# Kernel tuning notes

Measured on AMD Instinct MI355X. Metric: run time of the kernel, lower is better.

The kernel has to match this reference:

```python
import jax, jax.numpy as jnp
import numpy as np

N = 8192
E = 524288
IN_DIM = 128
HID = 256
OUT_DIM = 128
N_LAYERS = 3
N_HEADS = 4
HEAD_DIM = HID // N_HEADS


def setup_inputs() -> dict:
    key = jax.random.key(0)
    ks = jax.random.split(key, 12)
    s = 0.05
    return {
        "x": jax.random.normal(ks[0], (N, IN_DIM), dtype=jnp.float32),
        "edge_index": jax.random.randint(ks[1], (2, E), 0, N, dtype=jnp.int64),
        "W_in": jax.random.normal(ks[2], (HID, IN_DIM), dtype=jnp.float32) * s,
        "b_in": jnp.zeros((HID,), dtype=jnp.float32),
        "plasticity": jnp.ones((N_LAYERS,), dtype=jnp.float32),
        "synaptic": jnp.ones((N_LAYERS,), dtype=jnp.float32),
        "in_proj_w": jax.random.normal(ks[3], (3 * HID, HID), dtype=jnp.float32) * s,
        "in_proj_b": jnp.zeros((3 * HID,), dtype=jnp.float32),
        "out_proj_w": jax.random.normal(ks[4], (HID, HID), dtype=jnp.float32) * s,
        "out_proj_b": jnp.zeros((HID,), dtype=jnp.float32),
        "W_out": jax.random.normal(ks[5], (OUT_DIM, HID), dtype=jnp.float32) * s,
        "b_out": jnp.zeros((OUT_DIM,), dtype=jnp.float32),
    }


def _forward(x, edge_index, W_in, b_in, plasticity, synaptic,
             in_proj_w, in_proj_b, out_proj_w, out_proj_b, W_out, b_out):
    src, dst = edge_index[0], edge_index[1]  # x_j = x[src], aggregate at dst (source_to_target)
    x = x @ W_in.T + b_in  # [N, HID]
    for i in range(N_LAYERS):
        x = x * jax.nn.sigmoid(plasticity[i])
        # message: x_j * sigmoid(synaptic) (scalar edge weight); aggr='add'
        agg = jax.ops.segment_sum(x[src], dst, num_segments=N)  # gather-scatter-add
        x = jax.nn.leaky_relu(agg * jax.nn.sigmoid(synaptic[i]), negative_slope=0.01)
    # MultiheadAttention over all N nodes (seq_len=N, batch=1)
    qkv = x @ in_proj_w.T + in_proj_b  # [N, 3*HID]
    q, k, v = jnp.split(qkv, 3, axis=-1)
    q = q.reshape(N, N_HEADS, HEAD_DIM).transpose(1, 0, 2)  # [h, n, d]
    k = k.reshape(N, N_HEADS, HEAD_DIM).transpose(1, 0, 2)
    v = v.reshape(N, N_HEADS, HEAD_DIM).transpose(1, 0, 2)
    scores = jnp.einsum("hnd,hmd->hnm", q, k) / np.sqrt(HEAD_DIM).astype(np.float32)
    attn = jax.nn.softmax(scores, axis=-1)
    o = jnp.einsum("hnm,hmd->hnd", attn, v)  # [h, n, d]
    o = o.transpose(1, 0, 2).reshape(N, HID)
    x = o @ out_proj_w.T + out_proj_b
    return x @ W_out.T + b_out  # [N, OUT_DIM]


def reference(x, edge_index, W_in, b_in, plasticity, synaptic,
              in_proj_w, in_proj_b, out_proj_w, out_proj_b, W_out, b_out):
    return _forward(x, edge_index, W_in, b_in, plasticity, synaptic,
                    in_proj_w, in_proj_b, out_proj_w, out_proj_b, W_out, b_out)
```

## Files before the change

kernel.cpp:

```cpp
#include <hip/hip_runtime.h>
#include <hip/hip_bf16.h>
#include <float.h>

#define N_NODES 8192
#define NEDGE   524288
#define IND     128
#define HID     256
#define OUTD    128
#define NHEAD   4
#define HD      64

typedef short short8 __attribute__((ext_vector_type(8)));
typedef float f32x4  __attribute__((ext_vector_type(4)));
typedef float f32x16 __attribute__((ext_vector_type(16)));
typedef unsigned int u32x4 __attribute__((ext_vector_type(4)));

__device__ __forceinline__ float sigmoidf_(float x) { return 1.0f / (1.0f + expf(-x)); }

__device__ __forceinline__ unsigned short f2bf(float f) {
    __hip_bfloat16 b = __float2bfloat16(f);
    return __builtin_bit_cast(unsigned short, b);
}
__device__ __forceinline__ float bf2f(unsigned short u) {
    __hip_bfloat16 b = __builtin_bit_cast(__hip_bfloat16, u);
    return __bfloat162float(b);
}
__device__ __forceinline__ void split3(float x, unsigned short& a, unsigned short& b, unsigned short& c) {
    a = f2bf(x); float r = x - bf2f(a);
    b = f2bf(r); r = r - bf2f(b);
    c = f2bf(r);
}
__device__ __forceinline__ unsigned int cvtpk(float lo, float hi) {
    unsigned int r;
    asm("v_cvt_pk_bf16_f32 %0, %1, %2" : "=v"(r) : "v"(lo), "v"(hi));
    return r;
}
__device__ __forceinline__ void plswap(unsigned int& a, unsigned int& b) {
    asm volatile("v_permlane32_swap_b32 %0, %1" : "+v"(a), "+v"(b));
}
__device__ __forceinline__ void gll16(const void* g, void* l) {
    __builtin_amdgcn_global_load_lds(
        (const __attribute__((address_space(1))) void*)g,
        (__attribute__((address_space(3))) void*)l, 16, 0, 0);
}
__device__ __forceinline__ f32x16 mfma32(short8 a, short8 b, f32x16 c) {
    return __builtin_amdgcn_mfma_f32_32x32x16_bf16(a, b, c, 0, 0, 0);
}

__global__ __launch_bounds__(256) void gemm_bias_kernel(
    const float* __restrict__ A, const float* __restrict__ W,
    const float* __restrict__ bias, float* __restrict__ C,
    int M, int Nn, int K)
{
    __shared__ float As[128][33];
    __shared__ float Ws[64][33];
    const int t  = threadIdx.x;
    const int tx = t & 15, ty = t >> 4;
    const int m0 = blockIdx.x * 128, n0 = blockIdx.y * 64;
    const int alr = t >> 1, alc = (t & 1) * 16;
    const int wlr = t >> 2, wlc = (t & 3) * 8;

    float acc[8][4] = {};
    for (int kk = 0; kk < K; kk += 32) {
        const float* Ap = A + (size_t)(m0 + alr) * K + kk + alc;
        const float* Wp = W + (size_t)(n0 + wlr) * K + kk + wlc;
        float4 a0 = *(const float4*)(Ap);
        float4 a1 = *(const float4*)(Ap + 4);
        float4 a2 = *(const float4*)(Ap + 8);
        float4 a3 = *(const float4*)(Ap + 12);
        float4 w0 = *(const float4*)(Wp);
        float4 w1 = *(const float4*)(Wp + 4);
        __syncthreads();
        *(float4*)(&As[alr][alc + 0])  = a0;
        *(float4*)(&As[alr][alc + 4])  = a1;
        *(float4*)(&As[alr][alc + 8])  = a2;
        *(float4*)(&As[alr][alc + 12]) = a3;
        *(float4*)(&Ws[wlr][wlc + 0])  = w0;
        *(float4*)(&Ws[wlr][wlc + 4])  = w1;
        __syncthreads();
        #pragma unroll 4
        for (int k = 0; k < 32; ++k) {
            float a[8], w[4];
            #pragma unroll
            for (int i = 0; i < 8; ++i) a[i] = As[ty * 8 + i][k];
            #pragma unroll
            for (int j = 0; j < 4; ++j) w[j] = Ws[tx * 4 + j][k];
            #pragma unroll
            for (int i = 0; i < 8; ++i)
                #pragma unroll
                for (int j = 0; j < 4; ++j)
                    acc[i][j] += a[i] * w[j];
        }
    }
    #pragma unroll
    for (int i = 0; i < 8; ++i) {
        const int m = m0 + ty * 8 + i;
        #pragma unroll
        for (int j = 0; j < 4; ++j) {
            const int n = n0 + tx * 4 + j;
            C[(size_t)m * Nn + n] = acc[i][j] + bias[n];
        }
    }
}

__global__ void hist_kernel(const int* __restrict__ ei, int* __restrict__ deg)
{
    int e = blockIdx.x * blockDim.x + threadIdx.x;
    if (e < NEDGE) atomicAdd(&deg[ei[NEDGE + e]], 1);
}

__global__ __launch_bounds__(1024) void scan_kernel(
    const int* __restrict__ deg, int* __restrict__ row_ptr, int* __restrict__ cursor)
{
    __shared__ int sh[1024];
    const int t = threadIdx.x;
    int v[8]; int s = 0;
    #pragma unroll
    for (int i = 0; i < 8; ++i) { v[i] = deg[t * 8 + i]; s += v[i]; }
    sh[t] = s; __syncthreads();
    for (int off = 1; off < 1024; off <<= 1) {
        int add = (t >= off) ? sh[t - off] : 0;
        __syncthreads();
        sh[t] += add;
        __syncthreads();
    }
    int base = sh[t] - s;
    #pragma unroll
    for (int i = 0; i < 8; ++i) {
        row_ptr[t * 8 + i] = base;
        cursor[t * 8 + i]  = base;
        base += v[i];
    }
    if (t == 1023) row_ptr[N_NODES] = base;
}

__global__ void scatter_kernel(const int* __restrict__ ei, int* __restrict__ cursor,
                               int* __restrict__ esrc)
{
    int e = blockIdx.x * blockDim.x + threadIdx.x;
    if (e < NEDGE) {
        int d = ei[NEDGE + e];
        int p = atomicAdd(&cursor[d], 1);
        esrc[p] = ei[e];
    }
}

__global__ __launch_bounds__(256) void aggregate_kernel(
    const float* __restrict__ hin, float* __restrict__ hout,
    const int* __restrict__ row_ptr, const int* __restrict__ esrc,
    const float* __restrict__ plas, const float* __restrict__ syn, int layer)
{
    const int b = blockIdx.x;
    const int c = threadIdx.x;
    const int st = row_ptr[b], en = row_ptr[b + 1];
    float a0 = 0.f, a1 = 0.f, a2 = 0.f, a3 = 0.f;
    int e = st;
    for (; e + 4 <= en; e += 4) {
        int s0 = esrc[e], s1 = esrc[e + 1], s2 = esrc[e + 2], s3 = esrc[e + 3];
        a0 += hin[(size_t)s0 * HID + c];
        a1 += hin[(size_t)s1 * HID + c];
        a2 += hin[(size_t)s2 * HID + c];
        a3 += hin[(size_t)s3 * HID + c];
    }
    float acc = (a0 + a1) + (a2 + a3);
    for (; e < en; ++e) acc += hin[(size_t)esrc[e] * HID + c];
    const float scale = sigmoidf_(plas[layer]) * sigmoidf_(syn[layer]);
    float x = acc * scale;
    hout[(size_t)b * HID + c] = (x > 0.f) ? x : 0.01f * x;
}

__global__ __launch_bounds__(256) void split_kernel(
    const float* __restrict__ qkv,
    unsigned short* __restrict__ Kc0, unsigned short* __restrict__ Kc1,
    unsigned short* __restrict__ Kc2, unsigned short* __restrict__ Vt0)
{
    __shared__ unsigned short vts[64 * 80];
    const int h  = blockIdx.y;
    const int n0 = blockIdx.x * 64;
    const int t  = threadIdx.x;
    const int r  = t >> 2;
    const int n  = n0 + r;
    const int dc = (t & 3) * 16;

    {
        const float* kp = qkv + (size_t)n * 768 + 256 + h * 64 + dc;
        float kv[16];
        #pragma unroll
        for (int i = 0; i < 16; i += 4) {
            float4 f = *(const float4*)(kp + i);
            kv[i] = f.x; kv[i+1] = f.y; kv[i+2] = f.z; kv[i+3] = f.w;
        }
        #pragma unroll
        for (int half = 0; half < 2; ++half) {
            short8 c0, c1, c2;
            #pragma unroll
            for (int j = 0; j < 8; ++j) {
                unsigned short a, b, c;
                split3(kv[half * 8 + j], a, b, c);
                c0[j] = (short)a; c1[j] = (short)b; c2[j] = (short)c;
            }
            const int pos = ((dc >> 3) + half) ^ (n & 7);
            const size_t base = ((size_t)(h * 8192 + n)) * 64 + pos * 8;
            *(short8*)(Kc0 + base) = c0;
            *(short8*)(Kc1 + base) = c1;
            *(short8*)(Kc2 + base) = c2;
        }
    }
    {
        const float* vp = qkv + (size_t)n * 768 + 512 + h * 64 + dc;
        #pragma unroll
        for (int i = 0; i < 16; i += 4) {
            float4 f = *(const float4*)(vp + i);
            float vv[4] = {f.x, f.y, f.z, f.w};
            #pragma unroll
            for (int k2 = 0; k2 < 4; ++k2)
                vts[(dc + i + k2) * 80 + r] = f2bf(vv[k2]);
        }
    }
    __syncthreads();
    #pragma unroll
    for (int i = 0; i < 2; ++i) {
        const int q = t * 2 + i;
        const int d = q >> 3, nc = q & 7;
        short8 vv = *(const short8*)(&vts[d * 80 + nc * 8]);
        const size_t dst = ((size_t)(h * 64 + d)) * 8192 + n0 + ((nc ^ (d & 7)) * 8);
        *(short8*)(Vt0 + dst) = vv;
    }
}

__global__ __launch_bounds__(256, 2) void attn_mfma_kernel(
    const float* __restrict__ qkv,
    const unsigned short* __restrict__ Kc0, const unsigned short* __restrict__ Kc1,
    const unsigned short* __restrict__ Kc2, const unsigned short* __restrict__ Vt0,
    unsigned short* __restrict__ Op16, float* __restrict__ Ml)
{
    __shared__ __align__(16) char smem[65536];
    const int h    = blockIdx.y;
    const int quar = blockIdx.z;
    const int n0   = blockIdx.x * 256;
    const int t    = threadIdx.x;
    const int wv   = t >> 6;
    const int lane = t & 63;
    const int l31  = lane & 31, l5 = lane >> 5;
    const int qbase = n0 + wv * 64;

    short8 qf[2][3][4];
    #pragma unroll
    for (int qb = 0; qb < 2; ++qb) {
        #pragma unroll
        for (int ks = 0; ks < 4; ++ks) {
            const float* qp = qkv + (size_t)(qbase + qb * 32 + l31) * 768 + h * 64 + ks * 16 + l5 * 8;
            float4 qa = *(const float4*)qp, qb4 = *(const float4*)(qp + 4);
            float qv[8] = {qa.x, qa.y, qa.z, qa.w, qb4.x, qb4.y, qb4.z, qb4.w};
            #pragma unroll
            for (int j = 0; j < 8; ++j) {
                unsigned short a, b, c;
                split3(qv[j] * 0.125f, a, b, c);
                qf[qb][0][ks][j] = (short)a;
                qf[qb][1][ks][j] = (short)b;
                qf[qb][2][ks][j] = (short)c;
            }
        }
    }

    const unsigned short* cbase = (wv == 0) ? Kc0 : (wv == 1) ? Kc1 : (wv == 2) ? Kc2 : Vt0;
    const char* sgb[8];
    #pragma unroll
    for (int s = 0; s < 8; ++s) {
        const int row = s * 8 + (lane >> 3);
        if (wv < 3)
            sgb[s] = (const char*)(cbase + ((size_t)(h * 8192 + row)) * 64 + (lane & 7) * 8);
        else
            sgb[s] = (const char*)(cbase + ((size_t)(h * 64 + row)) * 8192 + (lane & 7) * 8);
    }
    const size_t ktstride = (wv < 3) ? 8192 : 128;
    const int ldsbase = wv * 8192;

    auto STAGE = [&](int ktg, int bb) {
        #pragma unroll
        for (int s = 0; s < 8; ++s)
            gll16(sgb[s] + (size_t)ktg * ktstride, &smem[bb * 32768 + ldsbase + s * 1024]);
    };

    f32x16 o[2][2];
    #pragma unroll
    for (int db = 0; db < 2; ++db)
        #pragma unroll
        for (int qb = 0; qb < 2; ++qb)
            #pragma unroll
            for (int r = 0; r < 16; ++r) o[db][qb][r] = 0.f;
    float mr[2] = {-FLT_MAX, -FLT_MAX};
    float ls[2] = {0.f, 0.f};

    const int kt0 = quar * 32;
    STAGE(kt0, 0);
    __syncthreads();

    for (int kt = 0; kt < 32; ++kt) {
        const int bb = kt & 1;
        if (kt < 31) STAGE(kt0 + kt + 1, bb ^ 1);
        const char* buf = &smem[bb * 32768];

        f32x16 s[2][2];
        #pragma unroll
        for (int kb = 0; kb < 2; ++kb)
            #pragma unroll
            for (int qb = 0; qb < 2; ++qb)
                #pragma unroll
                for (int r = 0; r < 16; ++r) s[kb][qb][r] = 0.f;

        __builtin_amdgcn_s_setprio(1);
        #pragma unroll
        for (int ks = 0; ks < 4; ++ks) {
            #pragma unroll
            for (int kb = 0; kb < 2; ++kb) {
                const int key = kb * 32 + l31;
                const int off = key * 128 + (((ks * 2 + l5) ^ (key & 7)) * 16);
                short8 k0 = *(const short8*)(buf + off);
                short8 k1 = *(const short8*)(buf + 8192 + off);
                short8 k2 = *(const short8*)(buf + 16384 + off);
                #pragma unroll
                for (int qb = 0; qb < 2; ++qb) {
                    f32x16 acc = s[kb][qb];
                    acc = mfma32(k0, qf[qb][2][ks], acc);
                    acc = mfma32(k1, qf[qb][1][ks], acc);
                    acc = mfma32(k2, qf[qb][0][ks], acc);
                    acc = mfma32(k0, qf[qb][1][ks], acc);
                    acc = mfma32(k1, qf[qb][0][ks], acc);
                    acc = mfma32(k0, qf[qb][0][ks], acc);
                    s[kb][qb] = acc;
                }
            }
        }
        __builtin_amdgcn_s_setprio(0);

        short8 pb[2][4];
        #pragma unroll
        for (int qb = 0; qb < 2; ++qb) {
            float mx = s[0][qb][0];
            #pragma unroll
            for (int r = 1; r < 16; ++r) mx = fmaxf(mx, s[0][qb][r]);
            #pragma unroll
            for (int r = 0; r < 16; ++r) mx = fmaxf(mx, s[1][qb][r]);
            mx = fmaxf(mx, __shfl_xor(mx, 32));
            if (__any(mx > mr[qb] + 8.f)) {
                const float mn = fmaxf(mr[qb], mx);
                const float alpha = __expf(mr[qb] - mn);
                mr[qb] = mn;
                ls[qb] *= alpha;
                o[0][qb] *= alpha;
                o[1][qb] *= alpha;
            }
            const float mkeep = mr[qb];
            float ps = 0.f;
            #pragma unroll
            for (int kb = 0; kb < 2; ++kb)
                #pragma unroll
                for (int r = 0; r < 16; ++r) {
                    float p = __expf(s[kb][qb][r] - mkeep);
                    s[kb][qb][r] = p;
                    ps += p;
                }
            ps += __shfl_xor(ps, 32);
            ls[qb] += ps;

            #pragma unroll
            for (int ks = 0; ks < 4; ++ks) {
                const int kb = ks >> 1, rb = (ks & 1) * 8;
                unsigned int A0 = cvtpk(s[kb][qb][rb + 0], s[kb][qb][rb + 1]);
                unsigned int A1 = cvtpk(s[kb][qb][rb + 2], s[kb][qb][rb + 3]);
                unsigned int B0 = cvtpk(s[kb][qb][rb + 4], s[kb][qb][rb + 5]);
                unsigned int B1 = cvtpk(s[kb][qb][rb + 6], s[kb][qb][rb + 7]);
                plswap(A0, B0);
                plswap(A1, B1);
                u32x4 pw; pw[0] = A0; pw[1] = A1; pw[2] = B0; pw[3] = B1;
                pb[qb][ks] = __builtin_bit_cast(short8, pw);
            }
        }

        __builtin_amdgcn_s_setprio(1);
        #pragma unroll
        for (int ks = 0; ks < 4; ++ks) {
            #pragma unroll
            for (int db = 0; db < 2; ++db) {
                const int d = db * 32 + l31;
                const int off = 24576 + d * 128 + (((ks * 2 + l5) ^ (d & 7)) * 16);
                short8 v = *(const short8*)(buf + off);
                o[db][0] = mfma32(v, pb[0][ks], o[db][0]);
                o[db][1] = mfma32(v, pb[1][ks], o[db][1]);
            }
        }
        __builtin_amdgcn_s_setprio(0);

        __syncthreads();
    }

    #pragma unroll
    for (int qb = 0; qb < 2; ++qb) {
        const int q = qbase + qb * 32 + l31;
        unsigned short* opq = Op16 + ((size_t)((quar * 4 + h) * 8192 + q)) * 64;
        #pragma unroll
        for (int db = 0; db < 2; ++db) {
            #pragma unroll
            for (int tq = 0; tq < 4; ++tq) {
                const int d0 = db * 32 + tq * 8 + l5 * 4;
                unsigned int w0 = cvtpk(o[db][qb][4 * tq + 0], o[db][qb][4 * tq + 1]);
                unsigned int w1 = cvtpk(o[db][qb][4 * tq + 2], o[db][qb][4 * tq + 3]);
                uint2 st = {w0, w1};
                *(uint2*)(opq + d0) = st;
            }
        }
        if (l5 == 0) {
            Ml[((size_t)(quar * 4 + h) * 2 + 0) * 8192 + q] = mr[qb];
            Ml[((size_t)(quar * 4 + h) * 2 + 1) * 8192 + q] = ls[qb];
        }
    }
}

__global__ __launch_bounds__(256) void combine_kernel(
    const unsigned short* __restrict__ Op16, const float* __restrict__ Ml,
    float* __restrict__ aO)
{
    const int idx = blockIdx.x * 256 + threadIdx.x;
    const int c = idx & 3;
    const int q = (idx >> 2) & 8191;
    const int h = idx >> 15;
    float m[4], l[4];
    float mg = -FLT_MAX;
    #pragma unroll
    for (int s = 0; s < 4; ++s) {
        m[s] = Ml[((size_t)(s * 4 + h) * 2 + 0) * 8192 + q];
        l[s] = Ml[((size_t)(s * 4 + h) * 2 + 1) * 8192 + q];
        mg = fmaxf(mg, m[s]);
    }
    float w[4], denom = 0.f;
    #pragma unroll
    for (int s = 0; s < 4; ++s) {
        w[s] = __expf(m[s] - mg);
        denom += l[s] * w[s];
    }
    const float inv = 1.f / denom;
    float acc[16] = {};
    #pragma unroll
    for (int s = 0; s < 4; ++s) {
        const unsigned short* p = Op16 + ((size_t)(s * 4 + h) * 8192 + q) * 64 + c * 16;
        short8 v0 = *(const short8*)(p);
        short8 v1 = *(const short8*)(p + 8);
        #pragma unroll
        for (int i = 0; i < 8; ++i) {
            acc[i]     += w[s] * bf2f((unsigned short)v0[i]);
            acc[i + 8] += w[s] * bf2f((unsigned short)v1[i]);
        }
    }
    float* dst = aO + (size_t)q * 256 + h * 64 + c * 16;
    #pragma unroll
    for (int i = 0; i < 4; ++i) {
        float4 r = { acc[4*i] * inv, acc[4*i+1] * inv, acc[4*i+2] * inv, acc[4*i+3] * inv };
        *(float4*)(dst + i * 4) = r;
    }
}

extern "C" void kernel_launch(void* const* d_in, const int* in_sizes, int n_in,
                              void* d_out, int out_size, void* d_ws, size_t ws_size,
                              hipStream_t stream)
{
    const float* x     = (const float*)d_in[0];
    const int*   ei    = (const int*)  d_in[1];
    const float* W_in  = (const float*)d_in[2];
    const float* b_in  = (const float*)d_in[3];
    const float* plas  = (const float*)d_in[4];
    const float* syn   = (const float*)d_in[5];
    const float* inpw  = (const float*)d_in[6];
    const float* inpb  = (const float*)d_in[7];
    const float* outpw = (const float*)d_in[8];
    const float* outpb = (const float*)d_in[9];
    const float* Wout  = (const float*)d_in[10];
    const float* bout  = (const float*)d_in[11];
    float* out = (float*)d_out;

    char* ws = (char*)d_ws;
    float* h    = (float*)(ws + 0);
    float* h2   = (float*)(ws + (8u  << 20));
    float* qkv  = (float*)(ws + (16u << 20));
    float* aO   = (float*)(ws + 0);
    float* tmp  = (float*)(ws + (48u << 20));
    unsigned short* Op16 = (unsigned short*)(ws + (40u << 20));
    unsigned short* Kc0 = (unsigned short*)(ws + 0);
    unsigned short* Kc1 = (unsigned short*)(ws + (4u  << 20));
    unsigned short* Kc2 = (unsigned short*)(ws + (8u  << 20));
    unsigned short* Vt0 = (unsigned short*)(ws + (12u << 20));
    int*   rowp = (int*)(ws + (56u << 20));
    int*   curs = (int*)(ws + (56u << 20) + 40960);
    int*   esrc = (int*)(ws + (56u << 20) + 81920);
    float* Ml   = (float*)(ws + (56u << 20) + 81920);

    hipMemsetAsync(curs, 0, N_NODES * sizeof(int), stream);
    hist_kernel<<<NEDGE / 256, 256, 0, stream>>>(ei, curs);
    scan_kernel<<<1, 1024, 0, stream>>>(curs, rowp, curs);
    scatter_kernel<<<NEDGE / 256, 256, 0, stream>>>(ei, curs, esrc);

    gemm_bias_kernel<<<dim3(N_NODES / 128, HID / 64), 256, 0, stream>>>(
        x, W_in, b_in, h, N_NODES, HID, IND);

    aggregate_kernel<<<N_NODES, 256, 0, stream>>>(h,  h2, rowp, esrc, plas, syn, 0);
    aggregate_kernel<<<N_NODES, 256, 0, stream>>>(h2, h,  rowp, esrc, plas, syn, 1);
    aggregate_kernel<<<N_NODES, 256, 0, stream>>>(h,  h2, rowp, esrc, plas, syn, 2);

    gemm_bias_kernel<<<dim3(N_NODES / 128, 768 / 64), 256, 0, stream>>>(
        h2, inpw, inpb, qkv, N_NODES, 768, HID);

    split_kernel<<<dim3(N_NODES / 64, NHEAD), 256, 0, stream>>>(
        qkv, Kc0, Kc1, Kc2, Vt0);

    attn_mfma_kernel<<<dim3(N_NODES / 256, NHEAD, 4), 256, 0, stream>>>(
        qkv, Kc0, Kc1, Kc2, Vt0, Op16, Ml);

    combine_kernel<<<512, 256, 0, stream>>>(Op16, Ml, aO);

    gemm_bias_kernel<<<dim3(N_NODES / 128, HID / 64), 256, 0, stream>>>(
        aO, outpw, outpb, tmp, N_NODES, HID, HID);
    gemm_bias_kernel<<<dim3(N_NODES / 128, OUTD / 64), 256, 0, stream>>>(
        tmp, Wout, bout, out, N_NODES, OUTD, HID);
}
```

Before: 590.1 us.

## Replace FP32 SIMT GEMMs with split-bf16 MFMA GEMMs and retile attention

Replaces the scalar FP32 GEMM kernel with an MFMA kernel that emulates FP32 through 3-way or 2-way bf16 splits, so the input, QKV, output-projection and final GEMMs run on matrix cores. The last aggregation, the combine step and the output projection now emit bf16 split components directly. The attention kernel is retiled to 128 queries per block with half the LDS, so three blocks fit per CU; it also uses exp2 with a folded log2e scale and a lazy max-rescale threshold. The V layout swizzle changes to match. The 2-term splits on the later GEMMs cost some accuracy, and the extra split passes add memory traffic.

```diff
diff --git a/kernel.cpp b/kernel.cpp
--- a/kernel.cpp
+++ b/kernel.cpp
@@ -11,6 +11,7 @@
 #define HD      64
 
 typedef short short8 __attribute__((ext_vector_type(8)));
+typedef short short4v __attribute__((ext_vector_type(4)));
 typedef float f32x4  __attribute__((ext_vector_type(4)));
 typedef float f32x16 __attribute__((ext_vector_type(16)));
 typedef unsigned int u32x4 __attribute__((ext_vector_type(4)));
@@ -30,6 +31,10 @@
     b = f2bf(r); r = r - bf2f(b);
     c = f2bf(r);
 }
+__device__ __forceinline__ void split2(float x, unsigned short& a, unsigned short& b) {
+    a = f2bf(x); float r = x - bf2f(a);
+    b = f2bf(r);
+}
 __device__ __forceinline__ unsigned int cvtpk(float lo, float hi) {
     unsigned int r;
     asm("v_cvt_pk_bf16_f32 %0, %1, %2" : "=v"(r) : "v"(lo), "v"(hi));
@@ -45,62 +50,6 @@
 }
 __device__ __forceinline__ f32x16 mfma32(short8 a, short8 b, f32x16 c) {
     return __builtin_amdgcn_mfma_f32_32x32x16_bf16(a, b, c, 0, 0, 0);
-}
-
-__global__ __launch_bounds__(256) void gemm_bias_kernel(
-    const float* __restrict__ A, const float* __restrict__ W,
-    const float* __restrict__ bias, float* __restrict__ C,
-    int M, int Nn, int K)
-{
-    __shared__ float As[128][33];
-    __shared__ float Ws[64][33];
-    const int t  = threadIdx.x;
-    const int tx = t & 15, ty = t >> 4;
-    const int m0 = blockIdx.x * 128, n0 = blockIdx.y * 64;
-    const int alr = t >> 1, alc = (t & 1) * 16;
-    const int wlr = t >> 2, wlc = (t & 3) * 8;
-
-    float acc[8][4] = {};
-    for (int kk = 0; kk < K; kk += 32) {
-        const float* Ap = A + (size_t)(m0 + alr) * K + kk + alc;
-        const float* Wp = W + (size_t)(n0 + wlr) * K + kk + wlc;
-        float4 a0 = *(const float4*)(Ap);
-        float4 a1 = *(const float4*)(Ap + 4);
-        float4 a2 = *(const float4*)(Ap + 8);
-        float4 a3 = *(const float4*)(Ap + 12);
-        float4 w0 = *(const float4*)(Wp);
-        float4 w1 = *(const float4*)(Wp + 4);
-        __syncthreads();
-        *(float4*)(&As[alr][alc + 0])  = a0;
-        *(float4*)(&As[alr][alc + 4])  = a1;
-        *(float4*)(&As[alr][alc + 8])  = a2;
-        *(float4*)(&As[alr][alc + 12]) = a3;
-        *(float4*)(&Ws[wlr][wlc + 0])  = w0;
-        *(float4*)(&Ws[wlr][wlc + 4])  = w1;
-        __syncthreads();
-        #pragma unroll 4
-        for (int k = 0; k < 32; ++k) {
-            float a[8], w[4];
-            #pragma unroll
-            for (int i = 0; i < 8; ++i) a[i] = As[ty * 8 + i][k];
-            #pragma unroll
-            for (int j = 0; j < 4; ++j) w[j] = Ws[tx * 4 + j][k];
-            #pragma unroll
-            for (int i = 0; i < 8; ++i)
-                #pragma unroll
-                for (int j = 0; j < 4; ++j)
-                    acc[i][j] += a[i] * w[j];
-        }
-    }
-    #pragma unroll
-    for (int i = 0; i < 8; ++i) {
-        const int m = m0 + ty * 8 + i;
-        #pragma unroll
-        for (int j = 0; j < 4; ++j) {
-            const int n = n0 + tx * 4 + j;
-            C[(size_t)m * Nn + n] = acc[i][j] + bias[n];
-        }
-    }
 }
 
 __global__ void hist_kernel(const int* __restrict__ ei, int* __restrict__ deg)
@@ -143,6 +92,27 @@
         int p = atomicAdd(&cursor[d], 1);
         esrc[p] = ei[e];
     }
+}
+
+__global__ __launch_bounds__(256) void split_x_kernel(
+    const float* __restrict__ x,
+    unsigned short* __restrict__ X0, unsigned short* __restrict__ X1,
+    unsigned short* __restrict__ X2)
+{
+    const int i = (blockIdx.x * 256 + threadIdx.x) * 8;
+    float4 a = *(const float4*)(x + i);
+    float4 b = *(const float4*)(x + i + 4);
+    float v[8] = {a.x, a.y, a.z, a.w, b.x, b.y, b.z, b.w};
+    short8 c0, c1, c2;
+    #pragma unroll
+    for (int j = 0; j < 8; ++j) {
+        unsigned short p, q, r;
+        split3(v[j], p, q, r);
+        c0[j] = (short)p; c1[j] = (short)q; c2[j] = (short)r;
+    }
+    *(short8*)(X0 + i) = c0;
+    *(short8*)(X1 + i) = c1;
+    *(short8*)(X2 + i) = c2;
 }
 
 __global__ __launch_bounds__(256) void aggregate_kernel(
@@ -167,6 +137,117 @@
     const float scale = sigmoidf_(plas[layer]) * sigmoidf_(syn[layer]);
     float x = acc * scale;
     hout[(size_t)b * HID + c] = (x > 0.f) ? x : 0.01f * x;
+}
+
+__global__ __launch_bounds__(256) void aggregate_split_kernel(
+    const float* __restrict__ hin,
+    unsigned short* __restrict__ H0, unsigned short* __restrict__ H1,
+    unsigned short* __restrict__ H2,
+    const int* __restrict__ row_ptr, const int* __restrict__ esrc,
+    const float* __restrict__ plas, const float* __restrict__ syn, int layer)
+{
+    const int b = blockIdx.x;
+    const int c = threadIdx.x;
+    const int st = row_ptr[b], en = row_ptr[b + 1];
+    float a0 = 0.f, a1 = 0.f, a2 = 0.f, a3 = 0.f;
+    int e = st;
+    for (; e + 4 <= en; e += 4) {
+        int s0 = esrc[e], s1 = esrc[e + 1], s2 = esrc[e + 2], s3 = esrc[e + 3];
+        a0 += hin[(size_t)s0 * HID + c];
+        a1 += hin[(size_t)s1 * HID + c];
+        a2 += hin[(size_t)s2 * HID + c];
+        a3 += hin[(size_t)s3 * HID + c];
+    }
+    float acc = (a0 + a1) + (a2 + a3);
+    for (; e < en; ++e) acc += hin[(size_t)esrc[e] * HID + c];
+    const float scale = sigmoidf_(plas[layer]) * sigmoidf_(syn[layer]);
+    float x = acc * scale;
+    x = (x > 0.f) ? x : 0.01f * x;
+    unsigned short p, q, r;
+    split3(x, p, q, r);
+    H0[(size_t)b * HID + c] = p;
+    H1[(size_t)b * HID + c] = q;
+    H2[(size_t)b * HID + c] = r;
+}
+
+template<int NT, int NA, bool SOUT>
+__global__ __launch_bounds__(256) void mfma_gemm_kernel(
+    const unsigned short* __restrict__ A0, const unsigned short* __restrict__ A1,
+    const unsigned short* __restrict__ A2,
+    const float* __restrict__ W, const float* __restrict__ bias,
+    float* __restrict__ Cf, unsigned short* __restrict__ C0, unsigned short* __restrict__ C1,
+    int M, int Nn, int K)
+{
+    const int t = threadIdx.x;
+    const int wv = t >> 6, lane = t & 63;
+    const int l31 = lane & 31, l5 = lane >> 5;
+    const int wm = wv & 1, wn = wv >> 1;
+    const int m0 = blockIdx.x * 64 + wm * 32;
+    const int n0 = blockIdx.y * 64 + wn * 32;
+    const int mrow = m0 + l31;
+    const int nrow = n0 + l31;
+
+    f32x16 o;
+    #pragma unroll
+    for (int r = 0; r < 16; ++r) o[r] = 0.f;
+
+    for (int k = 0; k < K; k += 16) {
+        const int kk = k + l5 * 8;
+        short8 af[NA];
+        af[0] = *(const short8*)(A0 + (size_t)mrow * K + kk);
+        af[1] = *(const short8*)(A1 + (size_t)mrow * K + kk);
+        if (NA > 2) af[2] = *(const short8*)(A2 + (size_t)mrow * K + kk);
+        const float* wp = W + (size_t)nrow * K + kk;
+        float4 w4a = *(const float4*)wp, w4b = *(const float4*)(wp + 4);
+        float wvle[8] = {w4a.x, w4a.y, w4a.z, w4a.w, w4b.x, w4b.y, w4b.z, w4b.w};
+        short8 wf[3];
+        #pragma unroll
+        for (int j = 0; j < 8; ++j) {
+            if (NT == 6) {
+                unsigned short a, b, c;
+                split3(wvle[j], a, b, c);
+                wf[0][j] = (short)a; wf[1][j] = (short)b; wf[2][j] = (short)c;
+            } else {
+                unsigned short a, b;
+                split2(wvle[j], a, b);
+                wf[0][j] = (short)a; wf[1][j] = (short)b;
+            }
+        }
+        if (NT == 6) {
+            o = mfma32(wf[0], af[2], o);
+            o = mfma32(wf[1], af[1], o);
+            o = mfma32(wf[2], af[0], o);
+            o = mfma32(wf[0], af[1], o);
+            o = mfma32(wf[1], af[0], o);
+            o = mfma32(wf[0], af[0], o);
+        } else {
+            o = mfma32(wf[0], af[1], o);
+            o = mfma32(wf[1], af[0], o);
+            o = mfma32(wf[0], af[0], o);
+        }
+    }
+
+    #pragma unroll
+    for (int g = 0; g < 4; ++g) {
+        const int nb = n0 + g * 8 + l5 * 4;
+        const float4 b4 = *(const float4*)(bias + nb);
+        float v0 = o[4 * g + 0] + b4.x;
+        float v1 = o[4 * g + 1] + b4.y;
+        float v2 = o[4 * g + 2] + b4.z;
+        float v3 = o[4 * g + 3] + b4.w;
+        if (!SOUT) {
+            float4 st = {v0, v1, v2, v3};
+            *(float4*)(Cf + (size_t)mrow * Nn + nb) = st;
+        } else {
+            unsigned short h0, h1, p0, p1, q0, q1, r0, r1;
+            split2(v0, h0, h1); split2(v1, p0, p1);
+            split2(v2, q0, q1); split2(v3, r0, r1);
+            short4v s0 = {(short)h0, (short)p0, (short)q0, (short)r0};
+            short4v s1 = {(short)h1, (short)p1, (short)q1, (short)r1};
+            *(short4v*)(C0 + (size_t)mrow * Nn + nb) = s0;
+            *(short4v*)(C1 + (size_t)mrow * Nn + nb) = s1;
+        }
+    }
 }
 
 __global__ __launch_bounds__(256) void split_kernel(
@@ -222,172 +303,152 @@
     for (int i = 0; i < 2; ++i) {
         const int q = t * 2 + i;
         const int d = q >> 3, nc = q & 7;
+        const int g = nc >> 2, c = nc & 3;
         short8 vv = *(const short8*)(&vts[d * 80 + nc * 8]);
-        const size_t dst = ((size_t)(h * 64 + d)) * 8192 + n0 + ((nc ^ (d & 7)) * 8);
+        const size_t dst = ((size_t)(h * 64 + d)) * 8192 + n0 + g * 32 + ((c ^ (d & 3)) * 8);
         *(short8*)(Vt0 + dst) = vv;
     }
 }
 
-__global__ __launch_bounds__(256, 2) void attn_mfma_kernel(
+__global__ __launch_bounds__(256, 3) void attn_mfma_kernel(
     const float* __restrict__ qkv,
     const unsigned short* __restrict__ Kc0, const unsigned short* __restrict__ Kc1,
     const unsigned short* __restrict__ Kc2, const unsigned short* __restrict__ Vt0,
     unsigned short* __restrict__ Op16, float* __restrict__ Ml)
 {
-    __shared__ __align__(16) char smem[65536];
+    __shared__ __align__(16) char smem[32768];
     const int h    = blockIdx.y;
     const int quar = blockIdx.z;
-    const int n0   = blockIdx.x * 256;
+    const int n0   = blockIdx.x * 128;
     const int t    = threadIdx.x;
     const int wv   = t >> 6;
     const int lane = t & 63;
     const int l31  = lane & 31, l5 = lane >> 5;
-    const int qbase = n0 + wv * 64;
-
-    short8 qf[2][3][4];
-    #pragma unroll
-    for (int qb = 0; qb < 2; ++qb) {
+    const int qbase = n0 + wv * 32;
+
+    const float QSC = 0.125f * 1.4426950408889634f;
+    short8 qf[3][4];
+    #pragma unroll
+    for (int ks = 0; ks < 4; ++ks) {
+        const float* qp = qkv + (size_t)(qbase + l31) * 768 + h * 64 + ks * 16 + l5 * 8;
+        float4 qa = *(const float4*)qp, qb4 = *(const float4*)(qp + 4);
+        float qv[8] = {qa.x, qa.y, qa.z, qa.w, qb4.x, qb4.y, qb4.z, qb4.w};
+        #pragma unroll
+        for (int j = 0; j < 8; ++j) {
+            unsigned short a, b, c;
+            split3(qv[j] * QSC, a, b, c);
+            qf[0][ks][j] = (short)a;
+            qf[1][ks][j] = (short)b;
+            qf[2][ks][j] = (short)c;
+        }
+    }
+
+    const char* sgb[4];
+    int ldso[4];
+    #pragma unroll
+    for (int i = 0; i < 4; ++i) {
+        const int s = wv * 4 + i;
+        if (s < 12) {
+            const int c = s >> 2, rb = s & 3;
+            const unsigned short* base = (c == 0) ? Kc0 : (c == 1) ? Kc1 : Kc2;
+            const int row = rb * 8 + (lane >> 3);
+            sgb[i] = (const char*)(base + ((size_t)(h * 8192 + quar * 2048 + row)) * 64 + (lane & 7) * 8);
+            ldso[i] = c * 4096 + rb * 1024;
+        } else {
+            const int v = s - 12;
+            const int d = v * 16 + (lane >> 2);
+            sgb[i] = (const char*)(Vt0 + ((size_t)(h * 64 + d)) * 8192 + quar * 2048 + (lane & 3) * 8);
+            ldso[i] = 12288 + v * 1024;
+        }
+    }
+    const size_t ktstride = (wv < 3) ? 4096 : 64;
+
+    auto STAGE = [&](int kt, int bb) {
+        #pragma unroll
+        for (int i = 0; i < 4; ++i)
+            gll16(sgb[i] + (size_t)kt * ktstride, &smem[bb * 16384 + ldso[i]]);
+    };
+
+    f32x16 o[2];
+    #pragma unroll
+    for (int db = 0; db < 2; ++db)
+        #pragma unroll
+        for (int r = 0; r < 16; ++r) o[db][r] = 0.f;
+    float mr = -FLT_MAX, ls = 0.f;
+
+    STAGE(0, 0);
+    __syncthreads();
+
+    for (int kt = 0; kt < 64; ++kt) {
+        const int bb = kt & 1;
+        if (kt < 63) STAGE(kt + 1, bb ^ 1);
+        const char* buf = &smem[bb * 16384];
+
+        f32x16 s;
+        #pragma unroll
+        for (int r = 0; r < 16; ++r) s[r] = 0.f;
+
+        __builtin_amdgcn_s_setprio(1);
         #pragma unroll
         for (int ks = 0; ks < 4; ++ks) {
-            const float* qp = qkv + (size_t)(qbase + qb * 32 + l31) * 768 + h * 64 + ks * 16 + l5 * 8;
-            float4 qa = *(const float4*)qp, qb4 = *(const float4*)(qp + 4);
-            float qv[8] = {qa.x, qa.y, qa.z, qa.w, qb4.x, qb4.y, qb4.z, qb4.w};
-            #pragma unroll
-            for (int j = 0; j < 8; ++j) {
-                unsigned short a, b, c;
-                split3(qv[j] * 0.125f, a, b, c);
-                qf[qb][0][ks][j] = (short)a;
-                qf[qb][1][ks][j] = (short)b;
-                qf[qb][2][ks][j] = (short)c;
-            }
-        }
-    }
-
-    const unsigned short* cbase = (wv == 0) ? Kc0 : (wv == 1) ? Kc1 : (wv == 2) ? Kc2 : Vt0;
-    const char* sgb[8];
-    #pragma unroll
-    for (int s = 0; s < 8; ++s) {
-        const int row = s * 8 + (lane >> 3);
-        if (wv < 3)
-            sgb[s] = (const char*)(cbase + ((size_t)(h * 8192 + row)) * 64 + (lane & 7) * 8);
-        else
-            sgb[s] = (const char*)(cbase + ((size_t)(h * 64 + row)) * 8192 + (lane & 7) * 8);
-    }
-    const size_t ktstride = (wv < 3) ? 8192 : 128;
-    const int ldsbase = wv * 8192;
-
-    auto STAGE = [&](int ktg, int bb) {
-        #pragma unroll
-        for (int s = 0; s < 8; ++s)
-            gll16(sgb[s] + (size_t)ktg * ktstride, &smem[bb * 32768 + ldsbase + s * 1024]);
-    };
-
-    f32x16 o[2][2];
-    #pragma unroll
-    for (int db = 0; db < 2; ++db)
-        #pragma unroll
-        for (int qb = 0; qb < 2; ++qb)
-            #pragma unroll
-            for (int r = 0; r < 16; ++r) o[db][qb][r] = 0.f;
-    float mr[2] = {-FLT_MAX, -FLT_MAX};
-    float ls[2] = {0.f, 0.f};
-
-    const int kt0 = quar * 32;
-    STAGE(kt0, 0);
-    __syncthreads();
-
-    for (int kt = 0; kt < 32; ++kt) {
-        const int bb = kt & 1;
-        if (kt < 31) STAGE(kt0 + kt + 1, bb ^ 1);
-        const char* buf = &smem[bb * 32768];
-
-        f32x16 s[2][2];
-        #pragma unroll
-        for (int kb = 0; kb < 2; ++kb)
-            #pragma unroll
-            for (int qb = 0; qb < 2; ++qb)
-                #pragma unroll
-                for (int r = 0; r < 16; ++r) s[kb][qb][r] = 0.f;
+            const int off = l31 * 128 + (((ks * 2 + l5) ^ (l31 & 7)) * 16);
+            short8 k0 = *(const short8*)(buf + off);
+            short8 k1 = *(const short8*)(buf + 4096 + off);
+            short8 k2 = *(const short8*)(buf + 8192 + off);
+            s = mfma32(k0, qf[2][ks], s);
+            s = mfma32(k1, qf[1][ks], s);
+            s = mfma32(k2, qf[0][ks], s);
+            s = mfma32(k0, qf[1][ks], s);
+            s = mfma32(k1, qf[0][ks], s);
+            s = mfma32(k0, qf[0][ks], s);
+        }
+        __builtin_amdgcn_s_setprio(0);
+
+        float mx = s[0];
+        #pragma unroll
+        for (int r = 1; r < 16; ++r) mx = fmaxf(mx, s[r]);
+        mx = fmaxf(mx, __shfl_xor(mx, 32));
+        if (__any(mx > mr + 12.0f)) {
+            const float mn = fmaxf(mr, mx);
+            const float alpha = exp2f(mr - mn);
+            mr = mn;
+            ls *= alpha;
+            o[0] *= alpha;
+            o[1] *= alpha;
+        }
+        float ps = 0.f;
+        #pragma unroll
+        for (int r = 0; r < 16; ++r) {
+            float p = exp2f(s[r] - mr);
+            s[r] = p;
+            ps += p;
+        }
+        ps += __shfl_xor(ps, 32);
+        ls += ps;
+
+        short8 pb[2];
+        #pragma unroll
+        for (int ks = 0; ks < 2; ++ks) {
+            const int rb = ks * 8;
+            unsigned int A0 = cvtpk(s[rb + 0], s[rb + 1]);
+            unsigned int A1 = cvtpk(s[rb + 2], s[rb + 3]);
+            unsigned int B0 = cvtpk(s[rb + 4], s[rb + 5]);
+            unsigned int B1 = cvtpk(s[rb + 6], s[rb + 7]);
+            plswap(A0, B0);
+            plswap(A1, B1);
+            u32x4 pw; pw[0] = A0; pw[1] = A1; pw[2] = B0; pw[3] = B1;
+            pb[ks] = __builtin_bit_cast(short8, pw);
+        }
 
         __builtin_amdgcn_s_setprio(1);
         #pragma unroll
-        for (int ks = 0; ks < 4; ++ks) {
-            #pragma unroll
-            for (int kb = 0; kb < 2; ++kb) {
-                const int key = kb * 32 + l31;
-                const int off = key * 128 + (((ks * 2 + l5) ^ (key & 7)) * 16);
-                short8 k0 = *(const short8*)(buf + off);
-                short8 k1 = *(const short8*)(buf + 8192 + off);
-                short8 k2 = *(const short8*)(buf + 16384 + off);
-                #pragma unroll
-                for (int qb = 0; qb < 2; ++qb) {
-                    f32x16 acc = s[kb][qb];
-                    acc = mfma32(k0, qf[qb][2][ks], acc);
-                    acc = mfma32(k1, qf[qb][1][ks], acc);
-                    acc = mfma32(k2, qf[qb][0][ks], acc);
-                    acc = mfma32(k0, qf[qb][1][ks], acc);
-                    acc = mfma32(k1, qf[qb][0][ks], acc);
-                    acc = mfma32(k0, qf[qb][0][ks], acc);
-                    s[kb][qb] = acc;
-                }
-            }
-        }
-        __builtin_amdgcn_s_setprio(0);
-
-        short8 pb[2][4];
-        #pragma unroll
-        for (int qb = 0; qb < 2; ++qb) {
-            float mx = s[0][qb][0];
-            #pragma unroll
-            for (int r = 1; r < 16; ++r) mx = fmaxf(mx, s[0][qb][r]);
-            #pragma unroll
-            for (int r = 0; r < 16; ++r) mx = fmaxf(mx, s[1][qb][r]);
-            mx = fmaxf(mx, __shfl_xor(mx, 32));
-            if (__any(mx > mr[qb] + 8.f)) {
-                const float mn = fmaxf(mr[qb], mx);
-                const float alpha = __expf(mr[qb] - mn);
-                mr[qb] = mn;
-                ls[qb] *= alpha;
-                o[0][qb] *= alpha;
-                o[1][qb] *= alpha;
-            }
-            const float mkeep = mr[qb];
-            float ps = 0.f;
-            #pragma unroll
-            for (int kb = 0; kb < 2; ++kb)
-                #pragma unroll
-                for (int r = 0; r < 16; ++r) {
-                    float p = __expf(s[kb][qb][r] - mkeep);
-                    s[kb][qb][r] = p;
-                    ps += p;
-                }
-            ps += __shfl_xor(ps, 32);
-            ls[qb] += ps;
-
-            #pragma unroll
-            for (int ks = 0; ks < 4; ++ks) {
-                const int kb = ks >> 1, rb = (ks & 1) * 8;
-                unsigned int A0 = cvtpk(s[kb][qb][rb + 0], s[kb][qb][rb + 1]);
-                unsigned int A1 = cvtpk(s[kb][qb][rb + 2], s[kb][qb][rb + 3]);
-                unsigned int B0 = cvtpk(s[kb][qb][rb + 4], s[kb][qb][rb + 5]);
-                unsigned int B1 = cvtpk(s[kb][qb][rb + 6], s[kb][qb][rb + 7]);
-                plswap(A0, B0);
-                plswap(A1, B1);
-                u32x4 pw; pw[0] = A0; pw[1] = A1; pw[2] = B0; pw[3] = B1;
-                pb[qb][ks] = __builtin_bit_cast(short8, pw);
-            }
-        }
-
-        __builtin_amdgcn_s_setprio(1);
-        #pragma unroll
-        for (int ks = 0; ks < 4; ++ks) {
+        for (int ks = 0; ks < 2; ++ks) {
             #pragma unroll
             for (int db = 0; db < 2; ++db) {
                 const int d = db * 32 + l31;
-                const int off = 24576 + d * 128 + (((ks * 2 + l5) ^ (d & 7)) * 16);
+                const int off = 12288 + d * 64 + (((ks * 2 + l5) ^ (d & 3)) * 16);
                 short8 v = *(const short8*)(buf + off);
-                o[db][0] = mfma32(v, pb[0][ks], o[db][0]);
-                o[db][1] = mfma32(v, pb[1][ks], o[db][1]);
+                o[db] = mfma32(v, pb[ks], o[db]);
             }
         }
         __builtin_amdgcn_s_setprio(0);
@@ -395,31 +456,30 @@
         __syncthreads();
     }
 
-    #pragma unroll
-    for (int qb = 0; qb < 2; ++qb) {
-        const int q = qbase + qb * 32 + l31;
+    {
+        const int q = qbase + l31;
         unsigned short* opq = Op16 + ((size_t)((quar * 4 + h) * 8192 + q)) * 64;
         #pragma unroll
         for (int db = 0; db < 2; ++db) {
             #pragma unroll
             for (int tq = 0; tq < 4; ++tq) {
                 const int d0 = db * 32 + tq * 8 + l5 * 4;
-                unsigned int w0 = cvtpk(o[db][qb][4 * tq + 0], o[db][qb][4 * tq + 1]);
-                unsigned int w1 = cvtpk(o[db][qb][4 * tq + 2], o[db][qb][4 * tq + 3]);
+                unsigned int w0 = cvtpk(o[db][4 * tq + 0], o[db][4 * tq + 1]);
+                unsigned int w1 = cvtpk(o[db][4 * tq + 2], o[db][4 * tq + 3]);
                 uint2 st = {w0, w1};
                 *(uint2*)(opq + d0) = st;
             }
         }
         if (l5 == 0) {
-            Ml[((size_t)(quar * 4 + h) * 2 + 0) * 8192 + q] = mr[qb];
-            Ml[((size_t)(quar * 4 + h) * 2 + 1) * 8192 + q] = ls[qb];
+            Ml[((size_t)(quar * 4 + h) * 2 + 0) * 8192 + q] = mr;
+            Ml[((size_t)(quar * 4 + h) * 2 + 1) * 8192 + q] = ls;
         }
     }
 }
 
 __global__ __launch_bounds__(256) void combine_kernel(
     const unsigned short* __restrict__ Op16, const float* __restrict__ Ml,
-    float* __restrict__ aO)
+    unsigned short* __restrict__ aO0, unsigned short* __restrict__ aO1)
 {
     const int idx = blockIdx.x * 256 + threadIdx.x;
     const int c = idx & 3;
@@ -436,7 +496,7 @@
     float w[4], denom = 0.f;
     #pragma unroll
     for (int s = 0; s < 4; ++s) {
-        w[s] = __expf(m[s] - mg);
+        w[s] = exp2f(m[s] - mg);
         denom += l[s] * w[s];
     }
     const float inv = 1.f / denom;
@@ -452,12 +512,25 @@
             acc[i + 8] += w[s] * bf2f((unsigned short)v1[i]);
         }
     }
-    float* dst = aO + (size_t)q * 256 + h * 64 + c * 16;
-    #pragma unroll
-    for (int i = 0; i < 4; ++i) {
-        float4 r = { acc[4*i] * inv, acc[4*i+1] * inv, acc[4*i+2] * inv, acc[4*i+3] * inv };
-        *(float4*)(dst + i * 4) = r;
-    }
+    unsigned short* d0 = aO0 + (size_t)q * 256 + h * 64 + c * 16;
+    unsigned short* d1 = aO1 + (size_t)q * 256 + h * 64 + c * 16;
+    short8 o0, o1;
+    #pragma unroll
+    for (int i = 0; i < 8; ++i) {
+        unsigned short a, b;
+        split2(acc[i] * inv, a, b);
+        o0[i] = (short)a; o1[i] = (short)b;
+    }
+    *(short8*)(d0) = o0;
+    *(short8*)(d1) = o1;
+    #pragma unroll
+    for (int i = 0; i < 8; ++i) {
+        unsigned short a, b;
+        split2(acc[i + 8] * inv, a, b);
+        o0[i] = (short)a; o1[i] = (short)b;
+    }
+    *(short8*)(d0 + 8) = o0;
+    *(short8*)(d1 + 8) = o1;
 }
 
 extern "C" void kernel_launch(void* const* d_in, const int* in_sizes, int n_in,
@@ -482,13 +555,21 @@
     float* h    = (float*)(ws + 0);
     float* h2   = (float*)(ws + (8u  << 20));
     float* qkv  = (float*)(ws + (16u << 20));
-    float* aO   = (float*)(ws + 0);
-    float* tmp  = (float*)(ws + (48u << 20));
+    unsigned short* xc0  = (unsigned short*)(ws + (16u << 20));
+    unsigned short* xc1  = (unsigned short*)(ws + (18u << 20));
+    unsigned short* xc2  = (unsigned short*)(ws + (20u << 20));
+    unsigned short* h2c0 = (unsigned short*)(ws + (8u  << 20));
+    unsigned short* h2c1 = (unsigned short*)(ws + (12u << 20));
+    unsigned short* h2c2 = (unsigned short*)(ws + (40u << 20));
+    unsigned short* Kc0  = (unsigned short*)(ws + 0);
+    unsigned short* Kc1  = (unsigned short*)(ws + (4u  << 20));
+    unsigned short* Kc2  = (unsigned short*)(ws + (8u  << 20));
+    unsigned short* Vt0  = (unsigned short*)(ws + (12u << 20));
     unsigned short* Op16 = (unsigned short*)(ws + (40u << 20));
-    unsigned short* Kc0 = (unsigned short*)(ws + 0);
-    unsigned short* Kc1 = (unsigned short*)(ws + (4u  << 20));
-    unsigned short* Kc2 = (unsigned short*)(ws + (8u  << 20));
-    unsigned short* Vt0 = (unsigned short*)(ws + (12u << 20));
+    unsigned short* aOc0 = (unsigned short*)(ws + 0);
+    unsigned short* aOc1 = (unsigned short*)(ws + (4u  << 20));
+    unsigned short* tmpc0 = (unsigned short*)(ws + (8u  << 20));
+    unsigned short* tmpc1 = (unsigned short*)(ws + (12u << 20));
     int*   rowp = (int*)(ws + (56u << 20));
     int*   curs = (int*)(ws + (56u << 20) + 40960);
     int*   esrc = (int*)(ws + (56u << 20) + 81920);
@@ -499,26 +580,28 @@
     scan_kernel<<<1, 1024, 0, stream>>>(curs, rowp, curs);
     scatter_kernel<<<NEDGE / 256, 256, 0, stream>>>(ei, curs, esrc);
 
-    gemm_bias_kernel<<<dim3(N_NODES / 128, HID / 64), 256, 0, stream>>>(
-        x, W_in, b_in, h, N_NODES, HID, IND);
+    split_x_kernel<<<(N_NODES * IND) / (256 * 8), 256, 0, stream>>>(x, xc0, xc1, xc2);
+    mfma_gemm_kernel<6, 3, false><<<dim3(N_NODES / 64, HID / 64), 256, 0, stream>>>(
+        xc0, xc1, xc2, W_in, b_in, h, nullptr, nullptr, N_NODES, HID, IND);
 
     aggregate_kernel<<<N_NODES, 256, 0, stream>>>(h,  h2, rowp, esrc, plas, syn, 0);
     aggregate_kernel<<<N_NODES, 256, 0, stream>>>(h2, h,  rowp, esrc, plas, syn, 1);
-    aggregate_kernel<<<N_NODES, 256, 0, stream>>>(h,  h2, rowp, esrc, plas, syn, 2);
-
-    gemm_bias_kernel<<<dim3(N_NODES / 128, 768 / 64), 256, 0, stream>>>(
-        h2, inpw, inpb, qkv, N_NODES, 768, HID);
+    aggregate_split_kernel<<<N_NODES, 256, 0, stream>>>(h, h2c0, h2c1, h2c2,
+                                                        rowp, esrc, plas, syn, 2);
+
+    mfma_gemm_kernel<6, 3, false><<<dim3(N_NODES / 64, 768 / 64), 256, 0, stream>>>(
+        h2c0, h2c1, h2c2, inpw, inpb, qkv, nullptr, nullptr, N_NODES, 768, HID);
 
     split_kernel<<<dim3(N_NODES / 64, NHEAD), 256, 0, stream>>>(
         qkv, Kc0, Kc1, Kc2, Vt0);
 
-    attn_mfma_kernel<<<dim3(N_NODES / 256, NHEAD, 4), 256, 0, stream>>>(
+    attn_mfma_kernel<<<dim3(N_NODES / 128, NHEAD, 4), 256, 0, stream>>>(
         qkv, Kc0, Kc1, Kc2, Vt0, Op16, Ml);
 
-    combine_kernel<<<512, 256, 0, stream>>>(Op16, Ml, aO);
-
-    gemm_bias_kernel<<<dim3(N_NODES / 128, HID / 64), 256, 0, stream>>>(
-        aO, outpw, outpb, tmp, N_NODES, HID, HID);
-    gemm_bias_kernel<<<dim3(N_NODES / 128, OUTD / 64), 256, 0, stream>>>(
-        tmp, Wout, bout, out, N_NODES, OUTD, HID);
-}
+    combine_kernel<<<512, 256, 0, stream>>>(Op16, Ml, aOc0, aOc1);
+
+    mfma_gemm_kernel<3, 2, true><<<dim3(N_NODES / 64, HID / 64), 256, 0, stream>>>(
+        aOc0, aOc1, nullptr, outpw, outpb, nullptr, tmpc0, tmpc1, N_NODES, HID, HID);
+    mfma_gemm_kernel<3, 2, false><<<dim3(N_NODES / 64, OUTD / 64), 256, 0, stream>>>(
+        tmpc0, tmpc1, nullptr, Wout, bout, out, nullptr, nullptr, N_NODES, OUTD, HID);
+}
```

Measured after the change: 602.7 us. 1.02x slower.
